# Optimization experiments

Hardware: AMD Instinct MI355X
Metric: run time of the kernel (lower is better)

Reference implementation:

```python
import jax, jax.numpy as jnp
import numpy as np


def setup_inputs() -> dict:
    key = jax.random.key(0)
    k1, k2, k3, k4 = jax.random.split(key, 4)
    B, N, F, H, C = 16, 4096, 8, 64, 256
    x = jax.random.normal(k1, (B, N, F, H), dtype=jnp.float32)
    W = jax.random.normal(k2, (H, 1), dtype=jnp.float32) / jnp.sqrt(jnp.float32(H))
    b = jax.random.normal(k3, (1,), dtype=jnp.float32) * 0.01
    segment_ids = jax.random.randint(k4, (N,), 0, C)
    return {"x": x, "W": W, "b": b, "segment_ids": segment_ids, "num_coarse": C}


def reference(x, W, b, segment_ids, num_coarse):
    # x: [B, N, F, H]; segment_ids: [N] -> coarse index; output: [B, C, F, H]
    B, N, Fdim, H = x.shape
    seg = segment_ids
    # node scores: Linear(hidden_dim, 1) on mean over feature axis -> [B, N]
    scores = (jnp.einsum('bnfh,ho->bn', x, W) / jnp.float32(Fdim)) + b[0]
    # numerically-stable per-segment softmax over fine nodes within each coarse group
    seg_max = jax.vmap(lambda s: jax.ops.segment_max(s, seg, num_segments=num_coarse))(scores)  # [B, C]
    e = jnp.exp(scores - seg_max[:, seg])                                                        # [B, N]
    denom = jax.vmap(lambda ee: jax.ops.segment_sum(ee, seg, num_segments=num_coarse))(e)        # [B, C]
    w = e / denom[:, seg]                                                                        # [B, N]
    # score-weighted segmented sum of fine features into coarse nodes
    pooled = jax.vmap(
        lambda wb, xb: jax.ops.segment_sum(wb[:, None, None] * xb, seg, num_segments=num_coarse)
    )(w, x)  # [B, C, F, H]
    return pooled
```

## Files before the change

### kernel.cpp

```cpp
#include <hip/hip_runtime.h>

#define B_ 16
#define N_ 4096
#define F_ 8
#define H_ 64
#define C_ 256
#define FH 512
#define CAP 256

__global__ __launch_bounds__(256, 6) void fused_pool_kernel(
    const float* __restrict__ x, const float* __restrict__ W,
    const float* __restrict__ bias, const int* __restrict__ seg,
    float* __restrict__ out)
{
    int c    = blockIdx.x & (C_ - 1);
    int b    = blockIdx.x >> 8;
    int t    = threadIdx.x;
    int wave = t >> 6;
    int lane = t & 63;

    __shared__ int    list[CAP];
    __shared__ int    cnt;
    __shared__ float4 acc_sh[4][128];
    __shared__ float  es_sh[4];

    if (t == 0) cnt = 0;
    __syncthreads();

    const int4* seg4 = (const int4*)seg;
#pragma unroll
    for (int k = 0; k < N_ / (256 * 4); k++) {
        int i4 = t + k * 256;
        int4 s4 = seg4[i4];
        int n0 = i4 * 4;
        if (s4.x == c) { int p = atomicAdd(&cnt, 1); if (p < CAP) list[p] = n0; }
        if (s4.y == c) { int p = atomicAdd(&cnt, 1); if (p < CAP) list[p] = n0 + 1; }
        if (s4.z == c) { int p = atomicAdd(&cnt, 1); if (p < CAP) list[p] = n0 + 2; }
        if (s4.w == c) { int p = atomicAdd(&cnt, 1); if (p < CAP) list[p] = n0 + 3; }
    }
    __syncthreads();
    int m = cnt;
    if (m > CAP) m = CAP;

    float4 w4 = *(const float4*)(W + ((4 * lane) & 63));
    float  bb = bias[0];

    const float4* x4 = (const float4*)x;
    size_t batch_base = (size_t)b * N_ * (FH / 4);

    float4 acc0 = {0, 0, 0, 0}, acc1 = {0, 0, 0, 0};
    float  esum = 0.0f;

    int j = wave;
    for (; j + 4 < m; j += 8) {
        int na = list[j], nb = list[j + 4];
        size_t ra = batch_base + (size_t)na * (FH / 4);
        size_t rb = batch_base + (size_t)nb * (FH / 4);
        float4 a0 = x4[ra + lane];
        float4 a1 = x4[ra + 64 + lane];
        float4 b0 = x4[rb + lane];
        float4 b1 = x4[rb + 64 + lane];

        float pa = (a0.x + a1.x) * w4.x + (a0.y + a1.y) * w4.y
                 + (a0.z + a1.z) * w4.z + (a0.w + a1.w) * w4.w;
        float pb = (b0.x + b1.x) * w4.x + (b0.y + b1.y) * w4.y
                 + (b0.z + b1.z) * w4.z + (b0.w + b1.w) * w4.w;
#pragma unroll
        for (int off = 32; off > 0; off >>= 1) {
            pa += __shfl_xor(pa, off, 64);
            pb += __shfl_xor(pb, off, 64);
        }
        float ea = __expf(pa * (1.0f / F_) + bb);
        float eb = __expf(pb * (1.0f / F_) + bb);
        esum += ea + eb;
        acc0.x += ea * a0.x + eb * b0.x; acc0.y += ea * a0.y + eb * b0.y;
        acc0.z += ea * a0.z + eb * b0.z; acc0.w += ea * a0.w + eb * b0.w;
        acc1.x += ea * a1.x + eb * b1.x; acc1.y += ea * a1.y + eb * b1.y;
        acc1.z += ea * a1.z + eb * b1.z; acc1.w += ea * a1.w + eb * b1.w;
    }
    if (j < m) {
        int na = list[j];
        size_t ra = batch_base + (size_t)na * (FH / 4);
        float4 a0 = x4[ra + lane];
        float4 a1 = x4[ra + 64 + lane];
        float pa = (a0.x + a1.x) * w4.x + (a0.y + a1.y) * w4.y
                 + (a0.z + a1.z) * w4.z + (a0.w + a1.w) * w4.w;
#pragma unroll
        for (int off = 32; off > 0; off >>= 1)
            pa += __shfl_xor(pa, off, 64);
        float ea = __expf(pa * (1.0f / F_) + bb);
        esum += ea;
        acc0.x += ea * a0.x; acc0.y += ea * a0.y; acc0.z += ea * a0.z; acc0.w += ea * a0.w;
        acc1.x += ea * a1.x; acc1.y += ea * a1.y; acc1.z += ea * a1.z; acc1.w += ea * a1.w;
    }

    acc_sh[wave][lane]      = acc0;
    acc_sh[wave][64 + lane] = acc1;
    if (lane == 0) es_sh[wave] = esum;
    __syncthreads();

    if (t < 128) {
        float es  = es_sh[0] + es_sh[1] + es_sh[2] + es_sh[3];
        float inv = (m > 0) ? 1.0f / es : 0.0f;
        float4 s0 = acc_sh[0][t];
        float4 s1 = acc_sh[1][t];
        float4 s2 = acc_sh[2][t];
        float4 s3 = acc_sh[3][t];
        float4 r;
        r.x = (s0.x + s1.x + s2.x + s3.x) * inv;
        r.y = (s0.y + s1.y + s2.y + s3.y) * inv;
        r.z = (s0.z + s1.z + s2.z + s3.z) * inv;
        r.w = (s0.w + s1.w + s2.w + s3.w) * inv;
        size_t ob = ((size_t)(b * C_ + c)) * (FH / 4);
        ((float4*)out)[ob + t] = r;
    }
}

extern "C" void kernel_launch(void* const* d_in, const int* in_sizes, int n_in,
                              void* d_out, int out_size, void* d_ws, size_t ws_size,
                              hipStream_t stream)
{
    const float* x    = (const float*)d_in[0];
    const float* W    = (const float*)d_in[1];
    const float* bias = (const float*)d_in[2];
    const int*   seg  = (const int*)d_in[3];
    float* out = (float*)d_out;

    fused_pool_kernel<<<B_ * C_, 256, 0, stream>>>(x, W, bias, seg, out);
}
```

Before: 200.7 us.

## Split each wave into half-wave row groups with four float4 loads per lane

Each wave now processes four rows per iteration, two per 32-lane half, with every lane loading four float4s from one row. That halves the dot-product shuffle reduction to five steps and doubles the memory-level parallelism per lane. Tail rows are handled with predication instead of a separate remainder path. A cross-half shuffle reduction is added before the shared-memory combine, and register use rises because there are four float4 accumulators plus eight loaded float4s, which may reduce occupancy.

```diff
diff --git a/kernel.cpp b/kernel.cpp
--- a/kernel.cpp
+++ b/kernel.cpp
@@ -7,6 +7,10 @@
 #define C_ 256
 #define FH 512
 #define CAP 256
+
+__device__ __forceinline__ float dot4(const float4 a, const float4 w) {
+    return (a.x * w.x + a.y * w.y) + (a.z * w.z + a.w * w.w);
+}
 
 __global__ __launch_bounds__(256, 6) void fused_pool_kernel(
     const float* __restrict__ x, const float* __restrict__ W,
@@ -18,10 +22,12 @@
     int t    = threadIdx.x;
     int wave = t >> 6;
     int lane = t & 63;
+    int grp  = lane >> 5;
+    int pos  = lane & 31;
 
     __shared__ int    list[CAP];
     __shared__ int    cnt;
-    __shared__ float4 acc_sh[4][128];
+    __shared__ float4 acc_sh[4][4][32];
     __shared__ float  es_sh[4];
 
     if (t == 0) cnt = 0;
@@ -42,70 +48,76 @@
     int m = cnt;
     if (m > CAP) m = CAP;
 
-    float4 w4 = *(const float4*)(W + ((4 * lane) & 63));
+    float4 w4 = *(const float4*)(W + ((4 * pos) & (H_ - 1)));
     float  bb = bias[0];
+    const float4* x4 = (const float4*)x;
+    size_t batch_base = (size_t)b * (N_ * (FH / 4));
 
-    const float4* x4 = (const float4*)x;
-    size_t batch_base = (size_t)b * N_ * (FH / 4);
-
-    float4 acc0 = {0, 0, 0, 0}, acc1 = {0, 0, 0, 0};
+    float4 acc0 = {0,0,0,0}, acc1 = {0,0,0,0}, acc2 = {0,0,0,0}, acc3 = {0,0,0,0};
     float  esum = 0.0f;
 
-    int j = wave;
-    for (; j + 4 < m; j += 8) {
-        int na = list[j], nb = list[j + 4];
-        size_t ra = batch_base + (size_t)na * (FH / 4);
-        size_t rb = batch_base + (size_t)nb * (FH / 4);
-        float4 a0 = x4[ra + lane];
-        float4 a1 = x4[ra + 64 + lane];
-        float4 b0 = x4[rb + lane];
-        float4 b1 = x4[rb + 64 + lane];
+    for (int base = wave * 4; base < m; base += 16) {
+        int r0 = base + grp;
+        int r1 = base + 2 + grp;
+        int a0 = (r0 < m), a1 = (r1 < m);
+        int cr0 = a0 ? r0 : (m - 1);
+        int cr1 = a1 ? r1 : (m - 1);
+        const float4* p0 = x4 + (batch_base + ((size_t)list[cr0] << 7) + pos);
+        const float4* p1 = x4 + (batch_base + ((size_t)list[cr1] << 7) + pos);
 
-        float pa = (a0.x + a1.x) * w4.x + (a0.y + a1.y) * w4.y
-                 + (a0.z + a1.z) * w4.z + (a0.w + a1.w) * w4.w;
-        float pb = (b0.x + b1.x) * w4.x + (b0.y + b1.y) * w4.y
-                 + (b0.z + b1.z) * w4.z + (b0.w + b1.w) * w4.w;
+        float4 v00, v01, v02, v03, v10, v11, v12, v13;
+        if (a0) { v00 = p0[0]; v01 = p0[32]; v02 = p0[64]; v03 = p0[96]; }
+        else    { v00 = v01 = v02 = v03 = make_float4(0.f, 0.f, 0.f, 0.f); }
+        if (a1) { v10 = p1[0]; v11 = p1[32]; v12 = p1[64]; v13 = p1[96]; }
+        else    { v10 = v11 = v12 = v13 = make_float4(0.f, 0.f, 0.f, 0.f); }
+
+        float d0 = (dot4(v00, w4) + dot4(v01, w4)) + (dot4(v02, w4) + dot4(v03, w4));
+        float d1 = (dot4(v10, w4) + dot4(v11, w4)) + (dot4(v12, w4) + dot4(v13, w4));
 #pragma unroll
-        for (int off = 32; off > 0; off >>= 1) {
-            pa += __shfl_xor(pa, off, 64);
-            pb += __shfl_xor(pb, off, 64);
+        for (int off = 16; off > 0; off >>= 1) {
+            d0 += __shfl_xor(d0, off);
+            d1 += __shfl_xor(d1, off);
         }
-        float ea = __expf(pa * (1.0f / F_) + bb);
-        float eb = __expf(pb * (1.0f / F_) + bb);
-        esum += ea + eb;
-        acc0.x += ea * a0.x + eb * b0.x; acc0.y += ea * a0.y + eb * b0.y;
-        acc0.z += ea * a0.z + eb * b0.z; acc0.w += ea * a0.w + eb * b0.w;
-        acc1.x += ea * a1.x + eb * b1.x; acc1.y += ea * a1.y + eb * b1.y;
-        acc1.z += ea * a1.z + eb * b1.z; acc1.w += ea * a1.w + eb * b1.w;
-    }
-    if (j < m) {
-        int na = list[j];
-        size_t ra = batch_base + (size_t)na * (FH / 4);
-        float4 a0 = x4[ra + lane];
-        float4 a1 = x4[ra + 64 + lane];
-        float pa = (a0.x + a1.x) * w4.x + (a0.y + a1.y) * w4.y
-                 + (a0.z + a1.z) * w4.z + (a0.w + a1.w) * w4.w;
-#pragma unroll
-        for (int off = 32; off > 0; off >>= 1)
-            pa += __shfl_xor(pa, off, 64);
-        float ea = __expf(pa * (1.0f / F_) + bb);
-        esum += ea;
-        acc0.x += ea * a0.x; acc0.y += ea * a0.y; acc0.z += ea * a0.z; acc0.w += ea * a0.w;
-        acc1.x += ea * a1.x; acc1.y += ea * a1.y; acc1.z += ea * a1.z; acc1.w += ea * a1.w;
+        float e0 = a0 ? __expf(d0 * (1.0f / F_) + bb) : 0.0f;
+        float e1 = a1 ? __expf(d1 * (1.0f / F_) + bb) : 0.0f;
+        esum += e0 + e1;
+        acc0.x += e0 * v00.x + e1 * v10.x; acc0.y += e0 * v00.y + e1 * v10.y;
+        acc0.z += e0 * v00.z + e1 * v10.z; acc0.w += e0 * v00.w + e1 * v10.w;
+        acc1.x += e0 * v01.x + e1 * v11.x; acc1.y += e0 * v01.y + e1 * v11.y;
+        acc1.z += e0 * v01.z + e1 * v11.z; acc1.w += e0 * v01.w + e1 * v11.w;
+        acc2.x += e0 * v02.x + e1 * v12.x; acc2.y += e0 * v02.y + e1 * v12.y;
+        acc2.z += e0 * v02.z + e1 * v12.z; acc2.w += e0 * v02.w + e1 * v12.w;
+        acc3.x += e0 * v03.x + e1 * v13.x; acc3.y += e0 * v03.y + e1 * v13.y;
+        acc3.z += e0 * v03.z + e1 * v13.z; acc3.w += e0 * v03.w + e1 * v13.w;
     }
 
-    acc_sh[wave][lane]      = acc0;
-    acc_sh[wave][64 + lane] = acc1;
-    if (lane == 0) es_sh[wave] = esum;
+    acc0.x += __shfl_xor(acc0.x, 32); acc0.y += __shfl_xor(acc0.y, 32);
+    acc0.z += __shfl_xor(acc0.z, 32); acc0.w += __shfl_xor(acc0.w, 32);
+    acc1.x += __shfl_xor(acc1.x, 32); acc1.y += __shfl_xor(acc1.y, 32);
+    acc1.z += __shfl_xor(acc1.z, 32); acc1.w += __shfl_xor(acc1.w, 32);
+    acc2.x += __shfl_xor(acc2.x, 32); acc2.y += __shfl_xor(acc2.y, 32);
+    acc2.z += __shfl_xor(acc2.z, 32); acc2.w += __shfl_xor(acc2.w, 32);
+    acc3.x += __shfl_xor(acc3.x, 32); acc3.y += __shfl_xor(acc3.y, 32);
+    acc3.z += __shfl_xor(acc3.z, 32); acc3.w += __shfl_xor(acc3.w, 32);
+    esum  += __shfl_xor(esum, 32);
+
+    if (lane < 32) {
+        acc_sh[wave][0][pos] = acc0;
+        acc_sh[wave][1][pos] = acc1;
+        acc_sh[wave][2][pos] = acc2;
+        acc_sh[wave][3][pos] = acc3;
+        if (lane == 0) es_sh[wave] = esum;
+    }
     __syncthreads();
 
     if (t < 128) {
+        int kk = t >> 5, pp = t & 31;
         float es  = es_sh[0] + es_sh[1] + es_sh[2] + es_sh[3];
         float inv = (m > 0) ? 1.0f / es : 0.0f;
-        float4 s0 = acc_sh[0][t];
-        float4 s1 = acc_sh[1][t];
-        float4 s2 = acc_sh[2][t];
-        float4 s3 = acc_sh[3][t];
+        float4 s0 = acc_sh[0][kk][pp];
+        float4 s1 = acc_sh[1][kk][pp];
+        float4 s2 = acc_sh[2][kk][pp];
+        float4 s3 = acc_sh[3][kk][pp];
         float4 r;
         r.x = (s0.x + s1.x + s2.x + s3.x) * inv;
         r.y = (s0.y + s1.y + s2.y + s3.y) * inv;
```

Result: no change. 201.8 us (+0.6%).
